# Kernel optimization log

Measured on AMD Instinct MI355X. Metric: run time of the kernel, lower is better.

Reference implementation:

```python
import jax, jax.numpy as jnp
import numpy as np

C = 256  # channels
SHAPES = [(8, C, 80, 80), (8, C, 40, 40), (8, C, 20, 20), (8, C, 10, 10)]
EPS = 1e-8  # torch cosine_similarity eps


def _nearest_resize(x, H, W):
    # Matches F.interpolate(mode='nearest'): src_idx = floor(dst_idx * in/out)
    b, c, h, w = x.shape
    rows = (jnp.arange(H) * h) // H
    cols = (jnp.arange(W) * w) // W
    return x[:, :, rows[:, None], cols[None, :]]


def setup_inputs() -> dict:
    key = jax.random.key(0)
    ks = jax.random.split(key, 12)
    d = {}
    for i, s in enumerate(SHAPES):
        d[f"f{i}"] = jax.random.normal(ks[i], s, dtype=jnp.float32)
        d[f"w{i}"] = jax.random.normal(ks[4 + i], (C, C), dtype=jnp.float32) / jnp.sqrt(jnp.float32(C))
        d[f"b{i}"] = jax.random.normal(ks[8 + i], (C,), dtype=jnp.float32) * 0.01
    return d


def reference(f0, f1, f2, f3, w0, w1, w2, w3, b0, b1, b2, b3):
    feats = [f0, f1, f2, f3]
    ws = [w0, w1, w2, w3]
    bs = [b0, b1, b2, b3]
    H = max(f.shape[2] for f in feats)
    W = max(f.shape[3] for f in feats)
    proj = []
    for f, w, b in zip(feats, ws, bs):
        # 1x1 conv == per-pixel GEMM over channels
        p = jnp.einsum('bchw,oc->bohw', f, w) + b[None, :, None, None]
        if p.shape[2] != H or p.shape[3] != W:
            p = _nearest_resize(p, H, W)
        proj.append(p)
    B = proj[0].shape[0]
    N = len(proj)
    x = jnp.stack(proj, axis=1).reshape(B, N, C, H * W)  # [B,N,C,L]
    # Pairwise cosine similarity along channel dim at each spatial location,
    # then mean over locations (vectorized form of the O(N^2) torch loop).
    dot = jnp.einsum('bicl,bjcl->bijl', x, x)            # [B,N,N,L]
    nrm = jnp.sqrt(jnp.einsum('bicl,bicl->bil', x, x))   # [B,N,L]
    denom = jnp.maximum(nrm[:, :, None, :] * nrm[:, None, :, :], EPS)
    attn = (dot / denom).mean(axis=-1)                   # [B,N,N]
    return jax.nn.softmax(attn, axis=-1)
```

## Files before the change

### kernel.cpp

```cpp
#include <hip/hip_runtime.h>


#define CCH 256
#define WPITCH 40

typedef __attribute__((ext_vector_type(8))) short short8;
typedef __attribute__((ext_vector_type(4))) short short4_;
typedef __attribute__((ext_vector_type(4))) float float4_;

__device__ inline short f2bf(float x) {
    union { float f; unsigned u; } c; c.f = x;
    unsigned u = c.u + 0x7FFFu + ((c.u >> 16) & 1u);
    return (short)(u >> 16);
}
__device__ inline float bf2f(short b) {
    union { unsigned u; float f; } c; c.u = ((unsigned)(unsigned short)b) << 16;
    return c.f;
}

__device__ inline void dma16(const void* g, void* l) {
    __builtin_amdgcn_global_load_lds(
        (const __attribute__((address_space(1))) void*)g,
        (__attribute__((address_space(3))) void*)l, 16, 0, 0);
}

__global__ __launch_bounds__(256) void proj_small(
    const float* __restrict__ f1, const float* __restrict__ f2,
    const float* __restrict__ f3,
    const float* __restrict__ w0, const float* __restrict__ w1,
    const float* __restrict__ w2, const float* __restrict__ w3,
    const float* __restrict__ b1, const float* __restrict__ b2,
    const float* __restrict__ b3,
    short* __restrict__ u1, short* __restrict__ u2, short* __restrict__ u3,
    short* __restrict__ wp)
{
    __shared__ __align__(16) short Wt[256 * WPITCH];
    __shared__ __align__(16) short Ft[64 * WPITCH];

    const int blk = blockIdx.x;
    const int t = threadIdx.x;

    if (blk >= 272) {
        int id = (blk - 272) * 256 + t;
        int ks = id >> 10;
        int rest = id & 1023;
        int mt = rest >> 6;
        int fl = rest & 63;
        int ln = fl & 15, qd = fl >> 4;
        const float* src = w0 + (size_t)(mt * 16 + ln) * CCH + ks * 32 + qd * 8;
        short8 v;
#pragma unroll
        for (int j = 0; j < 8; ++j) v[j] = f2bf(src[j]);
        *(short8*)(wp + (size_t)id * 8) = v;
        return;
    }

    int b, tile, L;
    const float* F; const float* Wg; const float* bias; short* U;
    if (blk < 200)      { int r = blk;       b = r / 25; tile = r % 25; L = 1600; F = f1; Wg = w1; bias = b1; U = u1; }
    else if (blk < 256) { int r = blk - 200; b = r / 7;  tile = r % 7;  L = 400;  F = f2; Wg = w2; bias = b2; U = u2; }
    else                { int r = blk - 256; b = r / 2;  tile = r % 2;  L = 100;  F = f3; Wg = w3; bias = b3; U = u3; }

    const int lane = t & 63;
    const int wav  = t >> 6;
    const int ln   = lane & 15;
    const int quad = lane >> 4;
    const int pixbase = tile * 64;
    const float* Fb = F + (size_t)b * CCH * L;

    const int wo = t >> 2;
    const int wk = (t & 3) * 8;
    const int fpix = t & 63;
    const int fchunk = t >> 6;
    const int gpix0 = pixbase + fpix;
    const bool pin = gpix0 < L;
    const int gl0 = pin ? gpix0 : 0;

    float4_ wbufA[4], wbufB[4];
    float fbuf[8];
    auto loadW = [&](int ks) {
#pragma unroll
        for (int p = 0; p < 4; ++p) {
            const float* srcp = Wg + (size_t)(p * 64 + wo) * CCH + ks * 32 + wk;
            wbufA[p] = *(const float4_*)srcp;
            wbufB[p] = *(const float4_*)(srcp + 4);
        }
    };
    auto loadF = [&](int ks) {
        const float* fs = Fb + (size_t)(ks * 32 + fchunk * 8) * L + gl0;
#pragma unroll
        for (int j = 0; j < 8; ++j) fbuf[j] = fs[(size_t)j * L];
    };

    float4_ acc[16];
#pragma unroll
    for (int i = 0; i < 16; ++i) acc[i] = (float4_){0.f, 0.f, 0.f, 0.f};

    loadW(0); loadF(0);
    for (int ks = 0; ks < 8; ++ks) {
        __syncthreads();
#pragma unroll
        for (int p = 0; p < 4; ++p) {
            short8 v;
#pragma unroll
            for (int e = 0; e < 4; ++e) { v[e] = f2bf(wbufA[p][e]); v[e + 4] = f2bf(wbufB[p][e]); }
            *(short8*)(&Wt[(p * 64 + wo) * WPITCH + wk]) = v;
        }
        {
            short8 v;
#pragma unroll
            for (int j = 0; j < 8; ++j) v[j] = pin ? f2bf(fbuf[j]) : (short)0;
            *(short8*)(&Ft[fpix * WPITCH + fchunk * 8]) = v;
        }
        __syncthreads();
        const int ksn = (ks + 1) & 7;
        loadW(ksn); loadF(ksn);

        short8 bfrag = *(const short8*)(&Ft[(wav * 16 + ln) * WPITCH + quad * 8]);
#pragma unroll
        for (int mt = 0; mt < 16; ++mt) {
            short8 afrag = *(const short8*)(&Wt[(mt * 16 + ln) * WPITCH + quad * 8]);
            acc[mt] = __builtin_amdgcn_mfma_f32_16x16x32_bf16(afrag, bfrag, acc[mt], 0, 0, 0);
        }
    }

    float ss = 0.f;
#pragma unroll
    for (int mt = 0; mt < 16; ++mt) {
        float4_ bv = *(const float4_*)(bias + mt * 16 + quad * 4);
#pragma unroll
        for (int r = 0; r < 4; ++r) { float v = acc[mt][r] + bv[r]; acc[mt][r] = v; ss += v * v; }
    }
    ss += __shfl_xor(ss, 16);
    ss += __shfl_xor(ss, 32);
    const float inv = 1.f / sqrtf(fmaxf(ss, 1e-24f));

    const int gpixw = pixbase + wav * 16 + ln;
    if (gpixw < L) {
        short* dst = U + ((size_t)b * L + gpixw) * CCH;
#pragma unroll
        for (int mt = 0; mt < 16; ++mt) {
            short4_ v;
#pragma unroll
            for (int r = 0; r < 4; ++r) v[r] = f2bf(acc[mt][r] * inv);
            *(short4_*)(dst + mt * 16 + quad * 4) = v;
        }
    }
}

__global__ __launch_bounds__(512) void proj0_dots(
    const float* __restrict__ F, const short* __restrict__ wp,
    const float* __restrict__ bias,
    const short* __restrict__ u1, const short* __restrict__ u2,
    const short* __restrict__ u3,
    float* __restrict__ partial)
{
    __shared__ __align__(16) char smem[65536];
    short* Wb0 = (short*)smem;
    short* Wb1 = (short*)(smem + 16384);
    float* Fb0 = (float*)(smem + 32768);
    float* Fb1 = (float*)(smem + 49152);
    short* S1 = (short*)smem;
    short* S2 = (short*)(smem + 16384);
    short* S3 = (short*)(smem + 20480);
    float* redF = (float*)(smem + 24576);
    float* redC = (float*)(smem + 24576 + 96);

    const int c  = blockIdx.x;
    const int b  = blockIdx.y;
    const int R  = c / 5, C = c - R * 5;
    const int t  = threadIdx.x;
    const int lane = t & 63;
    const int wav  = t >> 6;
    const int ln   = lane & 15;
    const int quad = lane >> 4;
    const float* Fbase = F + (size_t)b * CCH * 6400;

    auto dmaW = [&](int ks, int buf) {
        short* Wb = buf ? Wb1 : Wb0;
#pragma unroll
        for (int m = 0; m < 2; ++m) {
            const int k = wav * 2 + m;
            const short* g = wp + (size_t)ks * 8192 + k * 512 + lane * 8;
            dma16(g, Wb + k * 512);
        }
    };
    auto dmaF = [&](int ks, int buf) {
        float* Fb = buf ? Fb1 : Fb0;
#pragma unroll
        for (int m = 0; m < 2; ++m) {
            const int k = wav * 2 + m;
            const int chl = 2 * k + (lane >> 5);
            const int px4 = (lane & 31) * 4;
            const int gpx = (8 * R + (px4 >> 4)) * 80 + 16 * C + (px4 & 15);
            const float* g = Fbase + (size_t)(ks * 32 + chl) * 6400 + gpx;
            dma16(g, Fb + k * 256);
        }
    };

    float4_ acc[16];
#pragma unroll
    for (int i = 0; i < 16; ++i) acc[i] = (float4_){0.f, 0.f, 0.f, 0.f};

    const int pxme = wav * 16 + ln;

    dmaW(0, 0); dmaF(0, 0);
    for (int ks = 0; ks < 8; ++ks) {
        __syncthreads();
        if (ks < 7) { dmaW(ks + 1, (ks + 1) & 1); dmaF(ks + 1, (ks + 1) & 1); }
        const short* Wl = (ks & 1) ? Wb1 : Wb0;
        const float* Fl = (ks & 1) ? Fb1 : Fb0;
        short8 bfrag;
#pragma unroll
        for (int j = 0; j < 8; ++j)
            bfrag[j] = f2bf(Fl[(quad * 8 + j) * 128 + pxme]);
#pragma unroll
        for (int mt = 0; mt < 16; ++mt) {
            short8 afrag = *(const short8*)(Wl + mt * 512 + lane * 8);
            acc[mt] = __builtin_amdgcn_mfma_f32_16x16x32_bf16(afrag, bfrag, acc[mt], 0, 0, 0);
        }
    }

    float ss = 0.f;
#pragma unroll
    for (int mt = 0; mt < 16; ++mt) {
        float4_ bv = *(const float4_*)(bias + mt * 16 + quad * 4);
#pragma unroll
        for (int r = 0; r < 4; ++r) { float v = acc[mt][r] + bv[r]; acc[mt][r] = v; ss += v * v; }
    }
    ss += __shfl_xor(ss, 16);
    ss += __shfl_xor(ss, 32);
    const float inv = 1.f / sqrtf(fmaxf(ss, 1e-24f));

    __syncthreads();

    {
        const int p1 = t >> 4, ck = (t & 15) * 16;
        const int lr = p1 >> 3, lc = p1 & 7;
        const short* src = u1 + ((size_t)(b * 1600 + (4 * R + lr) * 40 + 8 * C + lc)) * CCH + ck;
        *(short8*)(&S1[p1 * 256 + ck])     = *(const short8*)src;
        *(short8*)(&S1[p1 * 256 + ck + 8]) = *(const short8*)(src + 8);
    }
    if (t < 128) {
        const int p2 = t >> 4, ck = (t & 15) * 16;
        const int lr = p2 >> 2, lc = p2 & 3;
        const short* src = u2 + ((size_t)(b * 400 + (2 * R + lr) * 20 + 4 * C + lc)) * CCH + ck;
        *(short8*)(&S2[p2 * 256 + ck])     = *(const short8*)src;
        *(short8*)(&S2[p2 * 256 + ck + 8]) = *(const short8*)(src + 8);
    }
    if (t < 32) {
        const int p3 = t >> 4, ck = (t & 15) * 16;
        const short* src = u3 + ((size_t)(b * 100 + R * 10 + 2 * C + p3)) * CCH + ck;
        *(short8*)(&S3[p3 * 256 + ck])     = *(const short8*)src;
        *(short8*)(&S3[p3 * 256 + ck + 8]) = *(const short8*)(src + 8);
    }
    __syncthreads();

    const int pr = pxme >> 4, pc = pxme & 15;
    const int c1l = (pr >> 1) * 8 + (pc >> 1);
    const int c2l = (pr >> 2) * 4 + (pc >> 2);
    const int c3l = pc >> 3;
    float d01 = 0.f, d02 = 0.f, d03 = 0.f;
#pragma unroll
    for (int mt = 0; mt < 16; ++mt) {
        const int ch = mt * 16 + quad * 4;
        short4_ v1 = *(const short4_*)(&S1[c1l * 256 + ch]);
        short4_ v2 = *(const short4_*)(&S2[c2l * 256 + ch]);
        short4_ v3 = *(const short4_*)(&S3[c3l * 256 + ch]);
#pragma unroll
        for (int r = 0; r < 4; ++r) {
            float a = acc[mt][r] * inv;
            d01 += a * bf2f(v1[r]);
            d02 += a * bf2f(v2[r]);
            d03 += a * bf2f(v3[r]);
        }
    }
    {
        float vals[3] = {d01, d02, d03};
#pragma unroll
        for (int p = 0; p < 3; ++p) {
            float v = vals[p];
            v += __shfl_xor(v, 1);  v += __shfl_xor(v, 2);  v += __shfl_xor(v, 4);
            v += __shfl_xor(v, 8);  v += __shfl_xor(v, 16); v += __shfl_xor(v, 32);
            if (lane == 0) redF[wav * 3 + p] = v;
        }
    }

    if (wav < 2) {
        const int p1 = wav * 16 + (lane >> 2);
        const int q  = lane & 3;
        const int lr = p1 >> 3, lc = p1 & 7;
        const int par2 = (lr >> 1) * 4 + (lc >> 1);
        const int par3 = lc >> 2;
        float e12 = 0.f, e13 = 0.f;
#pragma unroll
        for (int k = 0; k < 16; ++k) {
            short4_ a1 = *(const short4_*)(&S1[p1 * 256 + q * 64 + k * 4]);
            short4_ a2 = *(const short4_*)(&S2[par2 * 256 + q * 64 + k * 4]);
            short4_ a3 = *(const short4_*)(&S3[par3 * 256 + q * 64 + k * 4]);
#pragma unroll
            for (int r = 0; r < 4; ++r) {
                float x1 = bf2f(a1[r]);
                e12 += x1 * bf2f(a2[r]);
                e13 += x1 * bf2f(a3[r]);
            }
        }
        float ev[2] = {e12, e13};
#pragma unroll
        for (int p = 0; p < 2; ++p) {
            float v = ev[p];
            v += __shfl_xor(v, 1);  v += __shfl_xor(v, 2);  v += __shfl_xor(v, 4);
            v += __shfl_xor(v, 8);  v += __shfl_xor(v, 16); v += __shfl_xor(v, 32);
            if (lane == 0) redC[wav * 2 + p] = v;
        }
    } else if (wav == 2) {
        float e23 = 0.f;
        if (lane < 32) {
            const int p2 = lane >> 2;
            const int q  = lane & 3;
            const int par3 = (p2 & 3) >> 1;
#pragma unroll
            for (int k = 0; k < 16; ++k) {
                short4_ a2 = *(const short4_*)(&S2[p2 * 256 + q * 64 + k * 4]);
                short4_ a3 = *(const short4_*)(&S3[par3 * 256 + q * 64 + k * 4]);
#pragma unroll
                for (int r = 0; r < 4; ++r) e23 += bf2f(a2[r]) * bf2f(a3[r]);
            }
        }
        e23 += __shfl_xor(e23, 1);  e23 += __shfl_xor(e23, 2);  e23 += __shfl_xor(e23, 4);
        e23 += __shfl_xor(e23, 8);  e23 += __shfl_xor(e23, 16); e23 += __shfl_xor(e23, 32);
        if (lane == 0) redC[4] = e23;
    }
    __syncthreads();

    if (t < 6) {
        float v;
        if (t < 3) {
            v = 0.f;
#pragma unroll
            for (int w = 0; w < 8; ++w) v += redF[w * 3 + t];
        } else if (t == 3) v = redC[0] + redC[2];
        else if (t == 4)   v = redC[1] + redC[3];
        else               v = redC[4];
        partial[((size_t)b * 6 + t) * 50 + c] = v;
    }
}

__global__ void softmax4(const float* __restrict__ partial, float* __restrict__ out) {
    int t = threadIdx.x;
    if (t >= 128) return;
    int b = t >> 4, i = (t >> 2) & 3, j = t & 3;
    float a[4];
#pragma unroll
    for (int jj = 0; jj < 4; ++jj) {
        if (jj == i) { a[jj] = 1.0f; continue; }
        int lo = i < jj ? i : jj;
        int hi = i < jj ? jj : i;
        int pidx;
        if (lo == 0) pidx = hi - 1;
        else if (lo == 1) pidx = 1 + hi;
        else pidx = 5;
        const float* pp = partial + ((size_t)b * 6 + pidx) * 50;
        float s = 0.f;
        for (int k = 0; k < 50; ++k) s += pp[k];
        int rf = 80 >> lo;
        a[jj] = s / (float)(rf * rf);
    }
    float m = fmaxf(fmaxf(a[0], a[1]), fmaxf(a[2], a[3]));
    float e0 = expf(a[0] - m), e1 = expf(a[1] - m), e2 = expf(a[2] - m), e3 = expf(a[3] - m);
    float sum = e0 + e1 + e2 + e3;
    float ev = (j == 0) ? e0 : (j == 1) ? e1 : (j == 2) ? e2 : e3;
    out[t] = ev / sum;
}

extern "C" void kernel_launch(void* const* d_in, const int* in_sizes, int n_in,
                              void* d_out, int out_size, void* d_ws, size_t ws_size,
                              hipStream_t stream) {
    const float* f[4]  = {(const float*)d_in[0], (const float*)d_in[3],
                          (const float*)d_in[6], (const float*)d_in[9]};
    const float* w[4]  = {(const float*)d_in[1], (const float*)d_in[4],
                          (const float*)d_in[7], (const float*)d_in[10]};
    const float* bs[4] = {(const float*)d_in[2], (const float*)d_in[5],
                          (const float*)d_in[8], (const float*)d_in[11]};

    char* ws = (char*)d_ws;
    size_t off = 0;
    short* u1 = (short*)(ws + off); off += (size_t)8 * CCH * 1600 * sizeof(short);
    short* u2 = (short*)(ws + off); off += (size_t)8 * CCH * 400  * sizeof(short);
    short* u3 = (short*)(ws + off); off += (size_t)8 * CCH * 100  * sizeof(short);
    short* wp = (short*)(ws + off); off += (size_t)65536 * sizeof(short);
    float* partial = (float*)(ws + off);

    proj_small<<<304, 256, 0, stream>>>(f[1], f[2], f[3],
                                        w[0], w[1], w[2], w[3],
                                        bs[1], bs[2], bs[3],
                                        u1, u2, u3, wp);

    proj0_dots<<<dim3(50, 8), 512, 0, stream>>>(f[0], wp, bs[0],
                                                u1, u2, u3, partial);

    softmax4<<<1, 128, 0, stream>>>(partial, (float*)d_out);
}
```

Measured before the change: 156.1 us.

## Halve proj0_dots block to 256 threads with two pixel tiles per wave

```diff
diff --git a/kernel.cpp b/kernel.cpp
--- a/kernel.cpp
+++ b/kernel.cpp
@@ -3,6 +3,7 @@
 
 #define CCH 256
 #define WPITCH 40
+#define SPITCH 264
 
 typedef __attribute__((ext_vector_type(8))) short short8;
 typedef __attribute__((ext_vector_type(4))) short short4_;
@@ -148,7 +149,7 @@
     }
 }
 
-__global__ __launch_bounds__(512) void proj0_dots(
+__global__ __launch_bounds__(256) void proj0_dots(
     const float* __restrict__ F, const short* __restrict__ wp,
     const float* __restrict__ bias,
     const short* __restrict__ u1, const short* __restrict__ u2,
@@ -161,10 +162,10 @@
     float* Fb0 = (float*)(smem + 32768);
     float* Fb1 = (float*)(smem + 49152);
     short* S1 = (short*)smem;
-    short* S2 = (short*)(smem + 16384);
-    short* S3 = (short*)(smem + 20480);
-    float* redF = (float*)(smem + 24576);
-    float* redC = (float*)(smem + 24576 + 96);
+    short* S2 = (short*)(smem + 16896);
+    short* S3 = (short*)(smem + 21120);
+    float* redF = (float*)(smem + 22176);
+    float* redC = (float*)(smem + 22224);
 
     const int c  = blockIdx.x;
     const int b  = blockIdx.y;
@@ -179,8 +180,8 @@
     auto dmaW = [&](int ks, int buf) {
         short* Wb = buf ? Wb1 : Wb0;
 #pragma unroll
-        for (int m = 0; m < 2; ++m) {
-            const int k = wav * 2 + m;
+        for (int m = 0; m < 4; ++m) {
+            const int k = wav * 4 + m;
             const short* g = wp + (size_t)ks * 8192 + k * 512 + lane * 8;
             dma16(g, Wb + k * 512);
         }
@@ -188,8 +189,8 @@
     auto dmaF = [&](int ks, int buf) {
         float* Fb = buf ? Fb1 : Fb0;
 #pragma unroll
-        for (int m = 0; m < 2; ++m) {
-            const int k = wav * 2 + m;
+        for (int m = 0; m < 4; ++m) {
+            const int k = wav * 4 + m;
             const int chl = 2 * k + (lane >> 5);
             const int px4 = (lane & 31) * 4;
             const int gpx = (8 * R + (px4 >> 4)) * 80 + 16 * C + (px4 & 15);
@@ -198,11 +199,15 @@
         }
     };
 
-    float4_ acc[16];
-#pragma unroll
-    for (int i = 0; i < 16; ++i) acc[i] = (float4_){0.f, 0.f, 0.f, 0.f};
-
-    const int pxme = wav * 16 + ln;
+    float4_ accA[16], accB[16];
+#pragma unroll
+    for (int i = 0; i < 16; ++i) {
+        accA[i] = (float4_){0.f, 0.f, 0.f, 0.f};
+        accB[i] = (float4_){0.f, 0.f, 0.f, 0.f};
+    }
+
+    const int pxA = wav * 32 + ln;
+    const int pxB = pxA + 16;
 
     dmaW(0, 0); dmaF(0, 0);
     for (int ks = 0; ks < 8; ++ks) {
@@ -210,69 +215,78 @@
         if (ks < 7) { dmaW(ks + 1, (ks + 1) & 1); dmaF(ks + 1, (ks + 1) & 1); }
         const short* Wl = (ks & 1) ? Wb1 : Wb0;
         const float* Fl = (ks & 1) ? Fb1 : Fb0;
-        short8 bfrag;
-#pragma unroll
-        for (int j = 0; j < 8; ++j)
-            bfrag[j] = f2bf(Fl[(quad * 8 + j) * 128 + pxme]);
+        short8 bfA, bfB;
+#pragma unroll
+        for (int j = 0; j < 8; ++j) {
+            bfA[j] = f2bf(Fl[(quad * 8 + j) * 128 + pxA]);
+            bfB[j] = f2bf(Fl[(quad * 8 + j) * 128 + pxB]);
+        }
 #pragma unroll
         for (int mt = 0; mt < 16; ++mt) {
             short8 afrag = *(const short8*)(Wl + mt * 512 + lane * 8);
-            acc[mt] = __builtin_amdgcn_mfma_f32_16x16x32_bf16(afrag, bfrag, acc[mt], 0, 0, 0);
-        }
-    }
-
-    float ss = 0.f;
+            accA[mt] = __builtin_amdgcn_mfma_f32_16x16x32_bf16(afrag, bfA, accA[mt], 0, 0, 0);
+            accB[mt] = __builtin_amdgcn_mfma_f32_16x16x32_bf16(afrag, bfB, accB[mt], 0, 0, 0);
+        }
+    }
+
+    float ssA = 0.f, ssB = 0.f;
 #pragma unroll
     for (int mt = 0; mt < 16; ++mt) {
         float4_ bv = *(const float4_*)(bias + mt * 16 + quad * 4);
 #pragma unroll
-        for (int r = 0; r < 4; ++r) { float v = acc[mt][r] + bv[r]; acc[mt][r] = v; ss += v * v; }
-    }
-    ss += __shfl_xor(ss, 16);
-    ss += __shfl_xor(ss, 32);
-    const float inv = 1.f / sqrtf(fmaxf(ss, 1e-24f));
+        for (int r = 0; r < 4; ++r) {
+            float vA = accA[mt][r] + bv[r]; accA[mt][r] = vA; ssA += vA * vA;
+            float vB = accB[mt][r] + bv[r]; accB[mt][r] = vB; ssB += vB * vB;
+        }
+    }
+    ssA += __shfl_xor(ssA, 16); ssA += __shfl_xor(ssA, 32);
+    ssB += __shfl_xor(ssB, 16); ssB += __shfl_xor(ssB, 32);
+    const float invA = 1.f / sqrtf(fmaxf(ssA, 1e-24f));
+    const float invB = 1.f / sqrtf(fmaxf(ssB, 1e-24f));
 
     __syncthreads();
 
     {
-        const int p1 = t >> 4, ck = (t & 15) * 16;
+        const int p1 = t >> 3, co = (t & 7) * 32;
         const int lr = p1 >> 3, lc = p1 & 7;
-        const short* src = u1 + ((size_t)(b * 1600 + (4 * R + lr) * 40 + 8 * C + lc)) * CCH + ck;
-        *(short8*)(&S1[p1 * 256 + ck])     = *(const short8*)src;
-        *(short8*)(&S1[p1 * 256 + ck + 8]) = *(const short8*)(src + 8);
-    }
-    if (t < 128) {
-        const int p2 = t >> 4, ck = (t & 15) * 16;
+        const short* src = u1 + ((size_t)(b * 1600 + (4 * R + lr) * 40 + 8 * C + lc)) * CCH + co;
+        short* dst = S1 + p1 * SPITCH + co;
+#pragma unroll
+        for (int j = 0; j < 4; ++j) *(short8*)(dst + j * 8) = *(const short8*)(src + j * 8);
+    }
+    if (t < 64) {
+        const int p2 = t >> 3, co = (t & 7) * 32;
         const int lr = p2 >> 2, lc = p2 & 3;
-        const short* src = u2 + ((size_t)(b * 400 + (2 * R + lr) * 20 + 4 * C + lc)) * CCH + ck;
-        *(short8*)(&S2[p2 * 256 + ck])     = *(const short8*)src;
-        *(short8*)(&S2[p2 * 256 + ck + 8]) = *(const short8*)(src + 8);
-    }
-    if (t < 32) {
-        const int p3 = t >> 4, ck = (t & 15) * 16;
-        const short* src = u3 + ((size_t)(b * 100 + R * 10 + 2 * C + p3)) * CCH + ck;
-        *(short8*)(&S3[p3 * 256 + ck])     = *(const short8*)src;
-        *(short8*)(&S3[p3 * 256 + ck + 8]) = *(const short8*)(src + 8);
+        const short* src = u2 + ((size_t)(b * 400 + (2 * R + lr) * 20 + 4 * C + lc)) * CCH + co;
+        short* dst = S2 + p2 * SPITCH + co;
+#pragma unroll
+        for (int j = 0; j < 4; ++j) *(short8*)(dst + j * 8) = *(const short8*)(src + j * 8);
+    }
+    if (t < 16) {
+        const int p3 = t >> 3, co = (t & 7) * 32;
+        const short* src = u3 + ((size_t)(b * 100 + R * 10 + 2 * C + p3)) * CCH + co;
+        short* dst = S3 + p3 * SPITCH + co;
+#pragma unroll
+        for (int j = 0; j < 4; ++j) *(short8*)(dst + j * 8) = *(const short8*)(src + j * 8);
     }
     __syncthreads();
 
-    const int pr = pxme >> 4, pc = pxme & 15;
-    const int c1l = (pr >> 1) * 8 + (pc >> 1);
-    const int c2l = (pr >> 2) * 4 + (pc >> 2);
-    const int c3l = pc >> 3;
+    const int c1l = wav * 8 + (ln >> 1);
+    const int c2l = (wav >> 1) * 4 + (ln >> 2);
+    const int c3l = ln >> 3;
     float d01 = 0.f, d02 = 0.f, d03 = 0.f;
 #pragma unroll
     for (int mt = 0; mt < 16; ++mt) {
         const int ch = mt * 16 + quad * 4;
-        short4_ v1 = *(const short4_*)(&S1[c1l * 256 + ch]);
-        short4_ v2 = *(const short4_*)(&S2[c2l * 256 + ch]);
-        short4_ v3 = *(const short4_*)(&S3[c3l * 256 + ch]);
+        short4_ v1 = *(const short4_*)(&S1[c1l * SPITCH + ch]);
+        short4_ v2 = *(const short4_*)(&S2[c2l * SPITCH + ch]);
+        short4_ v3 = *(const short4_*)(&S3[c3l * SPITCH + ch]);
 #pragma unroll
         for (int r = 0; r < 4; ++r) {
-            float a = acc[mt][r] * inv;
-            d01 += a * bf2f(v1[r]);
-            d02 += a * bf2f(v2[r]);
-            d03 += a * bf2f(v3[r]);
+            float s = accA[mt][r] * invA + accB[mt][r] * invB;
+            d01 += s * bf2f(v1[r]);
+            d02 += s * bf2f(v2[r]);
+            d03 += s * bf2f(v3[r]);
         }
     }
     {
@@ -295,9 +309,10 @@
         float e12 = 0.f, e13 = 0.f;
 #pragma unroll
         for (int k = 0; k < 16; ++k) {
-            short4_ a1 = *(const short4_*)(&S1[p1 * 256 + q * 64 + k * 4]);
-            short4_ a2 = *(const short4_*)(&S2[par2 * 256 + q * 64 + k * 4]);
-            short4_ a3 = *(const short4_*)(&S3[par3 * 256 + q * 64 + k * 4]);
+            const int co = k * 16 + q * 4;
+            short4_ a1 = *(const short4_*)(&S1[p1 * SPITCH + co]);
+            short4_ a2 = *(const short4_*)(&S2[par2 * SPITCH + co]);
+            short4_ a3 = *(const short4_*)(&S3[par3 * SPITCH + co]);
 #pragma unroll
             for (int r = 0; r < 4; ++r) {
                 float x1 = bf2f(a1[r]);
@@ -321,8 +336,9 @@
             const int par3 = (p2 & 3) >> 1;
 #pragma unroll
             for (int k = 0; k < 16; ++k) {
-                short4_ a2 = *(const short4_*)(&S2[p2 * 256 + q * 64 + k * 4]);
-                short4_ a3 = *(const short4_*)(&S3[par3 * 256 + q * 64 + k * 4]);
+                const int co = k * 16 + q * 4;
+                short4_ a2 = *(const short4_*)(&S2[p2 * SPITCH + co]);
+                short4_ a3 = *(const short4_*)(&S3[par3 * SPITCH + co]);
 #pragma unroll
                 for (int r = 0; r < 4; ++r) e23 += bf2f(a2[r]) * bf2f(a3[r]);
             }
@@ -338,7 +354,7 @@
         if (t < 3) {
             v = 0.f;
 #pragma unroll
-            for (int w = 0; w < 8; ++w) v += redF[w * 3 + t];
+            for (int w = 0; w < 4; ++w) v += redF[w * 3 + t];
         } else if (t == 3) v = redC[0] + redC[2];
         else if (t == 4)   v = redC[1] + redC[3];
         else               v = redC[4];
@@ -396,7 +412,7 @@
                                         bs[1], bs[2], bs[3],
                                         u1, u2, u3, wp);
 
-    proj0_dots<<<dim3(50, 8), 512, 0, stream>>>(f[0], wp, bs[0],
+    proj0_dots<<<dim3(50, 8), 256, 0, stream>>>(f[0], wp, bs[0],
                                                 u1, u2, u3, partial);
 
     softmax4<<<1, 128, 0, stream>>>(partial, (float*)d_out);
```

Result: no change. 155.7 us (-0.2%).
